# Kernel optimization log

Hardware: AMD Instinct MI355X
Metric: run time of the kernel (lower is better)

## Reference

```python
import jax, jax.numpy as jnp
import numpy as np

B, N, K, F, E = 2, 16384, 32, 64, 16


def setup_inputs() -> dict:
    key = jax.random.key(0)
    k1, k2, k3, k4 = jax.random.split(key, 4)
    nodes = jax.random.normal(k1, (B, N, F), dtype=jnp.float32)
    # neighbor list: for each (batch, node) a list of K neighbor node indices
    nlist = jax.random.randint(k2, (B, N, K), 0, N, dtype=jnp.int32)
    edges = jax.random.normal(k3, (B, N, K, E), dtype=jnp.float32)
    # learned weight: (node_feat, node_feat, edge_feat) as in build()
    w = jax.random.normal(k4, (F, F, E), dtype=jnp.float32) * 0.05
    return {"nodes": nodes, "nlist": nlist, "edges": edges, "w": w}


def reference(nodes, nlist, edges, w):
    # tf.gather_nd(nodes, nlist): gather neighbor features -> [B, N, K, F]
    batch_idx = jnp.arange(nodes.shape[0], dtype=nlist.dtype)[:, None, None]
    sliced = nodes[batch_idx, nlist]  # [B, N, K, F]
    # edge-conditioned contraction: edges[b,i,j,n] * sliced[b,i,j,l] * w[l,m,n]
    prod = jnp.einsum('bijn,bijl,lmn->bijm', edges, sliced, w)  # [B, N, K, F]
    # mean over the K neighbors (axis=2); activation is None
    reduced = jnp.mean(prod, axis=2)  # [B, N, F]
    return reduced
```

## Files before the change

kernel.cpp:

```cpp
#include <hip/hip_runtime.h>
#include <cstdint>
#include <cstddef>

#define LOGN 14

typedef __bf16 bf16x8 __attribute__((ext_vector_type(8)));
typedef float f32x4 __attribute__((ext_vector_type(4)));
typedef unsigned u32;

#define BARRIER() __builtin_amdgcn_s_barrier()
#define LGKM0()   __builtin_amdgcn_s_waitcnt(0xC07F)
#define SFENCE()  __builtin_amdgcn_sched_barrier(0)

__device__ __forceinline__ u32 fbits(float f) { return __builtin_bit_cast(u32, f); }
__device__ __forceinline__ u32 pkrne(float lo, float hi) {
  u32 a = fbits(lo); a = a + 0x7fffu + ((a >> 16) & 1u);
  u32 b = fbits(hi); b = b + 0x7fffu + ((b >> 16) & 1u);
  return (b & 0xffff0000u) | (a >> 16);
}


__global__ void prep_wt(const float* __restrict__ w, unsigned short* __restrict__ wt) {
  int idx = blockIdx.x * 256 + threadIdx.x;
  int m = idx >> 10, k = idx & 1023;
  int ch = k >> 3, wv = k & 7, t = ch >> 4, cc = ch & 15;
  int l = (cc << 2) + (t >> 1), n = ((t & 1) << 3) + wv;
  u32 u = fbits(w[l * 1024 + m * 16 + n] * 0.03125f);
  wt[idx] = (unsigned short)((u + 0x7fffu + ((u >> 16) & 1u)) >> 16);
}

__global__ void prep_nb(const float* __restrict__ nodes, unsigned short* __restrict__ nb) {
  int idx = blockIdx.x * 256 + threadIdx.x;
  const float4* p = (const float4*)nodes + ((size_t)idx << 1);
  float4 a = p[0], b = p[1];
  uint4 o{pkrne(a.x, a.y), pkrne(a.z, a.w), pkrne(b.x, b.y), pkrne(b.z, b.w)};
  *((uint4*)nb + idx) = o;
}

__device__ __forceinline__ bf16x8 mk_bw(const float* wp) {
  float v[8];
  #pragma unroll
  for (int i = 0; i < 8; ++i) v[i] = wp[i] * 0.03125f;
  uint4 pk{pkrne(v[0], v[1]), pkrne(v[2], v[3]), pkrne(v[4], v[5]), pkrne(v[6], v[7])};
  return __builtin_bit_cast(bf16x8, pk);
}

__global__ __launch_bounds__(256, 1)
void mp_fused(const int* __restrict__ nlist, const float* __restrict__ edges,
              const unsigned short* __restrict__ wt, const unsigned short* __restrict__ nb,
              float* __restrict__ out) {
  __shared__ u32 g_lds[2 * 16 * 512];

  const int tid = threadIdx.x;
  const int lane = tid & 63;
  const int wid = __builtin_amdgcn_readfirstlane(tid >> 6);
  const int q = lane >> 4, c = lane & 15;

  const int blk = blockIdx.x;
  const int xcd = blk & 7;
  const int batch = xcd >> 2;
  const int ordinal = ((blk >> 3) << 2) + (xcd & 3);
  const int wg0 = (batch << LOGN) + (ordinal << 6);
  const unsigned short* __restrict__ nbb = nb + ((size_t)batch << 20);

  const int nd0 = wid << 2;
  const int m = (wid << 4) + c;

  bf16x8 wtreg[32];
  {
    const unsigned short* wb = wt + ((size_t)m << 10) + (q << 3);
    #pragma unroll
    for (int s = 0; s < 32; ++s) wtreg[s] = *(const bf16x8*)(wb + (s << 5));
  }

  int4  NI[4][2];
  uint2 U[4][8];
  float E[4][8];

  auto issue_nl = [&](int g) {
    #pragma unroll
    for (int j = 0; j < 4; ++j) {
      const int* r = nlist + (((size_t)(g + nd0 + j)) << 5) + (q << 3);
      NI[j][0] = *(const int4*)r;
      NI[j][1] = *(const int4*)(r + 4);
    }
  };
  auto issue_se2 = [&](int g, int j0) {
    #pragma unroll
    for (int jj = 0; jj < 2; ++jj) {
      const int j = j0 + jj;
      const int ix[8] = {NI[j][0].x, NI[j][0].y, NI[j][0].z, NI[j][0].w,
                         NI[j][1].x, NI[j][1].y, NI[j][1].z, NI[j][1].w};
      #pragma unroll
      for (int i = 0; i < 8; ++i)
        U[j][i] = *(const uint2*)(nbb + ((size_t)(u32)ix[i] << 6) + (c << 2));
      const float* ep = edges + (((size_t)(g + nd0 + j)) << 9) + (q << 7) + c;
      #pragma unroll
      for (int i = 0; i < 8; ++i) E[j][i] = ep[i << 4];
    }
  };
  auto consume_all = [&](int bsel) {
    #pragma unroll
    for (int j = 0; j < 4; ++j) {
      const int p = nd0 + j;
      uint4 apk{pkrne(E[j][0], E[j][1]), pkrne(E[j][2], E[j][3]),
                pkrne(E[j][4], E[j][5]), pkrne(E[j][6], E[j][7])};
      const bf16x8 af = __builtin_bit_cast(bf16x8, apk);
      #pragma unroll
      for (int lt = 0; lt < 4; ++lt) {
        const u32 sel = (lt & 1) ? 0x07060302u : 0x05040100u;
        u32 p0, p1, p2, p3;
        if (lt & 2) {
          p0 = __builtin_amdgcn_perm(U[j][1].y, U[j][0].y, sel);
          p1 = __builtin_amdgcn_perm(U[j][3].y, U[j][2].y, sel);
          p2 = __builtin_amdgcn_perm(U[j][5].y, U[j][4].y, sel);
          p3 = __builtin_amdgcn_perm(U[j][7].y, U[j][6].y, sel);
        } else {
          p0 = __builtin_amdgcn_perm(U[j][1].x, U[j][0].x, sel);
          p1 = __builtin_amdgcn_perm(U[j][3].x, U[j][2].x, sel);
          p2 = __builtin_amdgcn_perm(U[j][5].x, U[j][4].x, sel);
          p3 = __builtin_amdgcn_perm(U[j][7].x, U[j][6].x, sel);
        }
        uint4 spk{p0, p1, p2, p3};
        f32x4 acc{0.f, 0.f, 0.f, 0.f};
        acc = __builtin_amdgcn_mfma_f32_16x16x32_bf16(af,
                __builtin_bit_cast(bf16x8, spk), acc, 0, 0, 0);
        const u32 lo = pkrne(acc[0], acc[1]);
        const u32 hi = pkrne(acc[2], acc[3]);
        const int chunk = (c + (((lt << 1) + (q >> 1)) << 4)) ^ (p & 7);
        *(uint2*)&g_lds[(bsel << 13) + (p << 9) + (chunk << 2) + ((q & 1) << 1)] =
            uint2{lo, hi};
      }
    }
  };
  auto store_out = [&](int g, const f32x4& ob) {
    #pragma unroll
    for (int r = 0; r < 4; ++r)
      out[((size_t)(g + (q << 2) + r) << 6) + m] = ob[r];
  };

  issue_nl(wg0);
  issue_se2(wg0, 0);
  issue_se2(wg0, 2);
  issue_nl(wg0 + 16);
  consume_all(0);
  LGKM0(); BARRIER();

  #pragma unroll
  for (int t = 0; t < 3; ++t) {
    const int gn = wg0 + ((t + 1) << 4);
    issue_se2(gn, 0);
    SFENCE();
    f32x4 ob{0.f, 0.f, 0.f, 0.f};
    #pragma unroll
    for (int s = 0; s < 16; ++s) {
      uint4 ar = *(const uint4*)&g_lds[((t & 1) << 13) + (c << 9) +
                                       ((((s << 2) + q) ^ (c & 7)) << 2)];
      ob = __builtin_amdgcn_mfma_f32_16x16x32_bf16(__builtin_bit_cast(bf16x8, ar),
                                                   wtreg[s], ob, 0, 0, 0);
    }
    issue_se2(gn, 2);
    if (t < 2) issue_nl(wg0 + ((t + 2) << 4));
    SFENCE();
    #pragma unroll
    for (int s = 16; s < 32; ++s) {
      uint4 ar = *(const uint4*)&g_lds[((t & 1) << 13) + (c << 9) +
                                       ((((s << 2) + q) ^ (c & 7)) << 2)];
      ob = __builtin_amdgcn_mfma_f32_16x16x32_bf16(__builtin_bit_cast(bf16x8, ar),
                                                   wtreg[s], ob, 0, 0, 0);
    }
    store_out(wg0 + (t << 4), ob);
    consume_all((t & 1) ^ 1);
    LGKM0(); BARRIER();
  }

  {
    f32x4 ob{0.f, 0.f, 0.f, 0.f};
    #pragma unroll
    for (int s = 0; s < 32; ++s) {
      uint4 ar = *(const uint4*)&g_lds[(1 << 13) + (c << 9) +
                                       ((((s << 2) + q) ^ (c & 7)) << 2)];
      ob = __builtin_amdgcn_mfma_f32_16x16x32_bf16(__builtin_bit_cast(bf16x8, ar),
                                                   wtreg[s], ob, 0, 0, 0);
    }
    store_out(wg0 + 48, ob);
  }
}

template <int MODE>
__global__ __launch_bounds__(256, 3)
void mp_kernel(const float* __restrict__ nodes, const int* __restrict__ nlist,
               const float* __restrict__ edges, const unsigned short* __restrict__ wt,
               const float* __restrict__ w, float* __restrict__ out) {
  __shared__ u32 g_lds[16 * 512];

  const int tid = threadIdx.x;
  const int lane = tid & 63;
  const int wid = __builtin_amdgcn_readfirstlane(tid >> 6);
  const int q = lane >> 4, c = lane & 15;

  const int blk = blockIdx.x;
  const int xcd = blk & 7;
  const int batch = xcd >> 2;
  const int ordinal = ((blk >> 3) << 2) + (xcd & 3);
  const int wg0 = (batch << LOGN) + (ordinal << 4);
  const float* __restrict__ nbase = nodes + ((size_t)batch << 20);

  const int nd0 = wid << 2;

  auto issue_nl = [&](int t, int4* ni) {
    const int* r = nlist + (((size_t)(wg0 + nd0 + t)) << 5) + (q << 3);
    ni[0] = *(const int4*)r;
    ni[1] = *(const int4*)(r + 4);
  };
  auto issue_se = [&](int t, const int4* ni, f32x4* R, float* Ee) {
    const int ix[8] = {ni[0].x, ni[0].y, ni[0].z, ni[0].w,
                       ni[1].x, ni[1].y, ni[1].z, ni[1].w};
    #pragma unroll
    for (int i = 0; i < 8; ++i)
      R[i] = *(const f32x4*)(nbase + ((size_t)(u32)ix[i] << 6) + (c << 2));
    const float* ep = edges + (((size_t)(wg0 + nd0 + t)) << 9) + (q << 7) + c;
    #pragma unroll
    for (int i = 0; i < 8; ++i) Ee[i] = ep[i << 4];
  };
  auto consume = [&](int p, const f32x4* R, const float* Ee) {
    uint4 apk{pkrne(Ee[0], Ee[1]), pkrne(Ee[2], Ee[3]),
              pkrne(Ee[4], Ee[5]), pkrne(Ee[6], Ee[7])};
    const bf16x8 af = __builtin_bit_cast(bf16x8, apk);
    #pragma unroll
    for (int lt = 0; lt < 4; ++lt) {
      uint4 spk{pkrne(R[0][lt], R[1][lt]), pkrne(R[2][lt], R[3][lt]),
                pkrne(R[4][lt], R[5][lt]), pkrne(R[6][lt], R[7][lt])};
      f32x4 acc{0.f, 0.f, 0.f, 0.f};
      acc = __builtin_amdgcn_mfma_f32_16x16x32_bf16(af,
              __builtin_bit_cast(bf16x8, spk), acc, 0, 0, 0);
      const u32 lo = pkrne(acc[0], acc[1]);
      const u32 hi = pkrne(acc[2], acc[3]);
      const int chunk = (c + (((lt << 1) + (q >> 1)) << 4)) ^ (p & 7);
      *(uint2*)&g_lds[(p << 9) + (chunk << 2) + ((q & 1) << 1)] = uint2{lo, hi};
    }
  };

  {
    int4 ni0[2], ni1[2];
    f32x4 R0[8], R1[8];
    float E0[8], E1[8];
    issue_nl(0, ni0);
    issue_nl(1, ni1);
    issue_se(0, ni0, R0, E0);
    issue_nl(2, ni0);
    issue_se(1, ni1, R1, E1);
    issue_nl(3, ni1);
    SFENCE();
    consume(nd0 + 0, R0, E0);
    issue_se(2, ni0, R0, E0);
    SFENCE();
    consume(nd0 + 1, R1, E1);
    issue_se(3, ni1, R1, E1);
    SFENCE();
    consume(nd0 + 2, R0, E0);
    consume(nd0 + 3, R1, E1);
  }

  LGKM0();
  BARRIER();

  const int m = (wid << 4) + c;
  f32x4 ob{0.f, 0.f, 0.f, 0.f};
  if constexpr (MODE >= 1) {
    const unsigned short* wb = wt + ((size_t)m << 10) + (q << 3);
    #pragma unroll 8
    for (int s = 0; s < 32; ++s) {
      uint4 ar = *(const uint4*)&g_lds[(c << 9) + ((((s << 2) + q) ^ (c & 7)) << 2)];
      ob = __builtin_amdgcn_mfma_f32_16x16x32_bf16(__builtin_bit_cast(bf16x8, ar),
                                                   *(const bf16x8*)(wb + (s << 5)),
                                                   ob, 0, 0, 0);
    }
  } else {
    #pragma unroll 4
    for (int s = 0; s < 32; ++s) {
      uint4 ar = *(const uint4*)&g_lds[(c << 9) + ((((s << 2) + q) ^ (c & 7)) << 2)];
      const int ch = (s << 2) + q;
      const int l = ((ch & 15) << 2) + (ch >> 5);
      const int n0 = ((ch >> 4) & 1) << 3;
      const float* wp = w + l * 1024 + m * 16 + n0;
      ob = __builtin_amdgcn_mfma_f32_16x16x32_bf16(__builtin_bit_cast(bf16x8, ar),
                                                   mk_bw(wp), ob, 0, 0, 0);
    }
  }

  #pragma unroll
  for (int r = 0; r < 4; ++r)
    out[((size_t)(wg0 + (q << 2) + r) << 6) + m] = ob[r];
}

extern "C" void kernel_launch(void* const* d_in, const int* in_sizes, int n_in,
                              void* d_out, int out_size, void* d_ws, size_t ws_size,
                              hipStream_t stream) {
  const float* nodes = (const float*)d_in[0];
  const int*   nlist = (const int*)d_in[1];
  const float* edges = (const float*)d_in[2];
  const float* w     = (const float*)d_in[3];
  float* out = (float*)d_out;

  const size_t WT_BYTES = 131072;
  const size_t NB_BYTES = (size_t)1 << 22;

  if (ws_size >= WT_BYTES + NB_BYTES) {
    unsigned short* wt = (unsigned short*)d_ws;
    unsigned short* nb = wt + 65536;
    prep_wt<<<256, 256, 0, stream>>>(w, wt);
    prep_nb<<<1024, 256, 0, stream>>>(nodes, nb);
    mp_fused<<<512, 256, 0, stream>>>(nlist, edges, wt, nb, out);
  } else if (ws_size >= WT_BYTES) {
    unsigned short* wt = (unsigned short*)d_ws;
    prep_wt<<<256, 256, 0, stream>>>(w, wt);
    mp_kernel<1><<<2048, 256, 0, stream>>>(nodes, nlist, edges, wt, w, out);
  } else {
    mp_kernel<0><<<2048, 256, 0, stream>>>(nodes, nlist, edges, nullptr, w, out);
  }
}
```

Before: 135.5 us.

## Use 512-thread blocks with split-K phase-B and LDS partial-sum reduction

Doubles the workgroup to 8 waves, each covering 32 nodes per step instead of 16, and splits the phase-B K dimension across two wave halves. Each half holds 16 weight fragments instead of 32, and the halves combine their partial sums through an LDS reduction before storing. The aim is to cut per-wave register pressure for the weights and raise parallelism and occupancy, which allows two blocks per CU. The cost is a larger LDS footprint, an extra barrier and an LDS round trip per output tile. Grid size is halved to match.

New measurement: 154.8 us. 14.2% more time.

```diff
diff --git a/kernel.cpp b/kernel.cpp
--- a/kernel.cpp
+++ b/kernel.cpp
@@ -45,32 +45,34 @@
   return __builtin_bit_cast(bf16x8, pk);
 }
 
-__global__ __launch_bounds__(256, 1)
+__global__ __launch_bounds__(512, 2)
 void mp_fused(const int* __restrict__ nlist, const float* __restrict__ edges,
               const unsigned short* __restrict__ wt, const unsigned short* __restrict__ nb,
               float* __restrict__ out) {
-  __shared__ u32 g_lds[2 * 16 * 512];
+  __shared__ u32 g_lds[2 * 16384 + 2048];
 
   const int tid = threadIdx.x;
   const int lane = tid & 63;
   const int wid = __builtin_amdgcn_readfirstlane(tid >> 6);
   const int q = lane >> 4, c = lane & 15;
+  const int mt = wid & 3;
+  const int kh = wid >> 2;
 
   const int blk = blockIdx.x;
   const int xcd = blk & 7;
   const int batch = xcd >> 2;
   const int ordinal = ((blk >> 3) << 2) + (xcd & 3);
-  const int wg0 = (batch << LOGN) + (ordinal << 6);
+  const int wg0 = (batch << LOGN) + (ordinal << 7);
   const unsigned short* __restrict__ nbb = nb + ((size_t)batch << 20);
 
   const int nd0 = wid << 2;
-  const int m = (wid << 4) + c;
-
-  bf16x8 wtreg[32];
+  const int m = (mt << 4) + c;
+
+  bf16x8 wtreg[16];
   {
-    const unsigned short* wb = wt + ((size_t)m << 10) + (q << 3);
-    #pragma unroll
-    for (int s = 0; s < 32; ++s) wtreg[s] = *(const bf16x8*)(wb + (s << 5));
+    const unsigned short* wb = wt + ((size_t)m << 10) + (kh << 9) + (q << 3);
+    #pragma unroll
+    for (int i = 0; i < 16; ++i) wtreg[i] = *(const bf16x8*)(wb + (i << 5));
   }
 
   int4  NI[4][2];
@@ -128,62 +130,71 @@
         const u32 lo = pkrne(acc[0], acc[1]);
         const u32 hi = pkrne(acc[2], acc[3]);
         const int chunk = (c + (((lt << 1) + (q >> 1)) << 4)) ^ (p & 7);
-        *(uint2*)&g_lds[(bsel << 13) + (p << 9) + (chunk << 2) + ((q & 1) << 1)] =
+        *(uint2*)&g_lds[(bsel << 14) + (p << 9) + (chunk << 2) + ((q & 1) << 1)] =
             uint2{lo, hi};
       }
     }
   };
-  auto store_out = [&](int g, const f32x4& ob) {
-    #pragma unroll
-    for (int r = 0; r < 4; ++r)
-      out[((size_t)(g + (q << 2) + r) << 6) + m] = ob[r];
+  auto phaseB_step = [&](int bsel, int i, f32x4& o0, f32x4& o1) {
+    const int s = (kh << 4) + i;
+    const int col = ((((s << 2) + q) ^ (c & 7)) << 2);
+    uint4 a0 = *(const uint4*)&g_lds[(bsel << 14) + (c << 9) + col];
+    uint4 a1 = *(const uint4*)&g_lds[(bsel << 14) + ((16 + c) << 9) + col];
+    o0 = __builtin_amdgcn_mfma_f32_16x16x32_bf16(__builtin_bit_cast(bf16x8, a0),
+                                                 wtreg[i], o0, 0, 0, 0);
+    o1 = __builtin_amdgcn_mfma_f32_16x16x32_bf16(__builtin_bit_cast(bf16x8, a1),
+                                                 wtreg[i], o1, 0, 0, 0);
+  };
+  auto reduce_store = [&](int g, f32x4& o0, f32x4& o1) {
+    const int sb = 32768 + (mt << 9) + (lane << 2);
+    if (kh) {
+      *(uint4*)&g_lds[sb]       = __builtin_bit_cast(uint4, o0);
+      *(uint4*)&g_lds[sb + 256] = __builtin_bit_cast(uint4, o1);
+    }
+    LGKM0(); BARRIER();
+    if (!kh) {
+      f32x4 p0 = __builtin_bit_cast(f32x4, *(const uint4*)&g_lds[sb]);
+      f32x4 p1 = __builtin_bit_cast(f32x4, *(const uint4*)&g_lds[sb + 256]);
+      o0 += p0; o1 += p1;
+      #pragma unroll
+      for (int r = 0; r < 4; ++r)
+        out[((size_t)(g + (q << 2) + r) << 6) + m] = o0[r];
+      #pragma unroll
+      for (int r = 0; r < 4; ++r)
+        out[((size_t)(g + 16 + (q << 2) + r) << 6) + m] = o1[r];
+    }
   };
 
   issue_nl(wg0);
   issue_se2(wg0, 0);
   issue_se2(wg0, 2);
-  issue_nl(wg0 + 16);
+  issue_nl(wg0 + 32);
   consume_all(0);
   LGKM0(); BARRIER();
 
   #pragma unroll
   for (int t = 0; t < 3; ++t) {
-    const int gn = wg0 + ((t + 1) << 4);
+    const int gn = wg0 + ((t + 1) << 5);
     issue_se2(gn, 0);
     SFENCE();
-    f32x4 ob{0.f, 0.f, 0.f, 0.f};
-    #pragma unroll
-    for (int s = 0; s < 16; ++s) {
-      uint4 ar = *(const uint4*)&g_lds[((t & 1) << 13) + (c << 9) +
-                                       ((((s << 2) + q) ^ (c & 7)) << 2)];
-      ob = __builtin_amdgcn_mfma_f32_16x16x32_bf16(__builtin_bit_cast(bf16x8, ar),
-                                                   wtreg[s], ob, 0, 0, 0);
-    }
+    f32x4 o0{0.f, 0.f, 0.f, 0.f}, o1{0.f, 0.f, 0.f, 0.f};
+    #pragma unroll
+    for (int i = 0; i < 8; ++i) phaseB_step(t & 1, i, o0, o1);
     issue_se2(gn, 2);
-    if (t < 2) issue_nl(wg0 + ((t + 2) << 4));
-    SFENCE();
-    #pragma unroll
-    for (int s = 16; s < 32; ++s) {
-      uint4 ar = *(const uint4*)&g_lds[((t & 1) << 13) + (c << 9) +
-                                       ((((s << 2) + q) ^ (c & 7)) << 2)];
-      ob = __builtin_amdgcn_mfma_f32_16x16x32_bf16(__builtin_bit_cast(bf16x8, ar),
-                                                   wtreg[s], ob, 0, 0, 0);
-    }
-    store_out(wg0 + (t << 4), ob);
+    if (t < 2) issue_nl(wg0 + ((t + 2) << 5));
+    SFENCE();
+    #pragma unroll
+    for (int i = 8; i < 16; ++i) phaseB_step(t & 1, i, o0, o1);
+    reduce_store(wg0 + (t << 5), o0, o1);
     consume_all((t & 1) ^ 1);
     LGKM0(); BARRIER();
   }
 
   {
-    f32x4 ob{0.f, 0.f, 0.f, 0.f};
-    #pragma unroll
-    for (int s = 0; s < 32; ++s) {
-      uint4 ar = *(const uint4*)&g_lds[(1 << 13) + (c << 9) +
-                                       ((((s << 2) + q) ^ (c & 7)) << 2)];
-      ob = __builtin_amdgcn_mfma_f32_16x16x32_bf16(__builtin_bit_cast(bf16x8, ar),
-                                                   wtreg[s], ob, 0, 0, 0);
-    }
-    store_out(wg0 + 48, ob);
+    f32x4 o0{0.f, 0.f, 0.f, 0.f}, o1{0.f, 0.f, 0.f, 0.f};
+    #pragma unroll
+    for (int i = 0; i < 16; ++i) phaseB_step(1, i, o0, o1);
+    reduce_store(wg0 + 96, o0, o1);
   }
 }
 
@@ -311,7 +322,7 @@
     unsigned short* nb = wt + 65536;
     prep_wt<<<256, 256, 0, stream>>>(w, wt);
     prep_nb<<<1024, 256, 0, stream>>>(nodes, nb);
-    mp_fused<<<512, 256, 0, stream>>>(nlist, edges, wt, nb, out);
+    mp_fused<<<256, 512, 0, stream>>>(nlist, edges, wt, nb, out);
   } else if (ws_size >= WT_BYTES) {
     unsigned short* wt = (unsigned short*)d_ws;
     prep_wt<<<256, 256, 0, stream>>>(w, wt);
```
